# Kernel optimization log

Hardware: AMD Instinct MI355X
Metric: run time of the kernel (lower is better)

## Reference

```python
import jax, jax.numpy as jnp
import numpy as np

FEATURE_COUNT = 40960
HIDDEN = 256
BATCH = 131072
BAG = 32  # active features per perspective (fixed-size bag)


def setup_inputs() -> dict:
    key = jax.random.key(0)
    ks = jax.random.split(key, 9)
    inp = {
        "indices_us": jax.random.randint(ks[0], (BATCH, BAG), 0, FEATURE_COUNT, dtype=jnp.int32),
        "indices_them": jax.random.randint(ks[1], (BATCH, BAG), 0, FEATURE_COUNT, dtype=jnp.int32),
        "emb_weight": jax.random.normal(ks[2], (FEATURE_COUNT, HIDDEN), dtype=jnp.float32) * 0.05,
        "l1_w": jax.random.normal(ks[3], (32, 2 * HIDDEN), dtype=jnp.float32) * 0.05,
        "l1_b": jax.random.normal(ks[4], (32,), dtype=jnp.float32) * 0.05,
        "l2_w": jax.random.normal(ks[5], (32, 32), dtype=jnp.float32) * 0.05,
        "l2_b": jax.random.normal(ks[6], (32,), dtype=jnp.float32) * 0.05,
        "out_w": jax.random.normal(ks[7], (1, 32), dtype=jnp.float32) * 0.05,
        "out_b": jax.random.normal(ks[8], (1,), dtype=jnp.float32) * 0.05,
    }
    return inp


def _clipped_relu(x):
    return jnp.clip(x, 0.0, 1.0)


def reference(indices_us, indices_them, emb_weight, l1_w, l1_b, l2_w, l2_b, out_w, out_b):
    # EmbeddingBag(mode='sum') with uniform bags of size BAG:
    # gather [B, BAG, H] then sum over bag dim -> [B, H]
    acc_us = emb_weight[indices_us].sum(axis=1)
    acc_them = emb_weight[indices_them].sum(axis=1)
    x = jnp.concatenate([acc_us, acc_them], axis=1)  # [B, 2H]
    x = _clipped_relu(x)
    x = _clipped_relu(x @ l1_w.T + l1_b)
    x = _clipped_relu(x @ l2_w.T + l2_b)
    return x @ out_w.T + out_b  # [B, 1]
```

## Files before the change

kernel.cpp:

```cpp
#include <hip/hip_runtime.h>
#include <hip/hip_fp16.h>


constexpr int kBatch  = 131072;
constexpr int kHidden = 256;
constexpr int kBag    = 32;
constexpr int kFeat   = 40960;

__device__ __forceinline__ float clip1(float x) {
  return fminf(fmaxf(x, 0.0f), 1.0f);
}

template <int D, int HALF>
__device__ __forceinline__ void rs_stage(float (&p)[32], int lane) {
  const bool up = (lane & D) != 0;
#pragma unroll
  for (int i = 0; i < HALF; ++i) {
    const float send = up ? p[i] : p[i + HALF];
    const float recv = __shfl_xor(send, D, 64);
    p[i] = (up ? p[i + HALF] : p[i]) + recv;
  }
}

__device__ __forceinline__ float reduce32(float (&p)[32], int lane) {
  rs_stage<32, 16>(p, lane);
  rs_stage<16, 8>(p, lane);
  rs_stage<8, 4>(p, lane);
  rs_stage<4, 2>(p, lane);
  rs_stage<2, 1>(p, lane);
  return p[0] + __shfl_xor(p[0], 1, 64);
}

__global__ void cvt_emb(const float4* __restrict__ src, uint2* __restrict__ dst) {
  const int n4 = kFeat * kHidden / 4;
  const int stride = gridDim.x * blockDim.x;
  for (int i = blockIdx.x * blockDim.x + threadIdx.x; i < n4; i += stride) {
    const float4 v = src[i];
    union { __half2 h[2]; uint2 u; } P;
    P.h[0] = __floats2half2_rn(v.x, v.y);
    P.h[1] = __floats2half2_rn(v.z, v.w);
    dst[i] = P.u;
  }
}

constexpr int kBlocksH = 1024;
constexpr int kTpb     = 256;
constexpr int kWpb     = kTpb / 64;
constexpr int kElemsH  = kBatch / (kBlocksH * kWpb);
static_assert(kBatch % (kBlocksH * kWpb) == 0);

__device__ __forceinline__ void acc8(float (&a)[8], const uint4 v) {
  union { uint4 u; __half2 h[4]; } U;
  U.u = v;
#pragma unroll
  for (int q = 0; q < 4; ++q) {
    const float2 f = __half22float2(U.h[q]);
    a[2 * q + 0] += f.x;
    a[2 * q + 1] += f.y;
  }
}

__global__ __launch_bounds__(kTpb, 4) void nnue_fwd_h(
    const int* __restrict__ idx_us, const int* __restrict__ idx_th,
    const __half* __restrict__ embh, const float* __restrict__ w1,
    const float* __restrict__ b1, const float* __restrict__ w2,
    const float* __restrict__ b2, const float* __restrict__ wo,
    const float* __restrict__ bo, float* __restrict__ out) {
  __shared__ __align__(16) __half sW1h[32 * 512];
  __shared__ __align__(16) float sY1[kWpb][32];

  const int t = threadIdx.x;
  {
    const float4* src = (const float4*)w1;
#pragma unroll
    for (int c = 0; c < 16; ++c) {
      const float4 v = src[t * 16 + c];
      __half2* d = (__half2*)&sW1h[t * 64 + 4 * c];
      d[0] = __floats2half2_rn(v.x, v.y);
      d[1] = __floats2half2_rn(v.z, v.w);
    }
  }
  __syncthreads();

  const int lane   = t & 63;
  const int wlocal = t >> 6;
  const int wid    = blockIdx.x * kWpb + wlocal;
  const int myj    = lane >> 1;
  const int j2     = lane & 31;
  const int half31 = lane & 31;
  const bool hiHalf = lane >= 32;

  const float b1r  = b1[myj];
  const float b2r  = b2[j2];
  const float wor  = wo[j2];
  const float outb = bo[0];
  float w2r[32];
#pragma unroll
  for (int k = 0; k < 32; ++k) w2r[k] = w2[j2 * 32 + k];

  for (int e = 0; e < kElemsH; ++e) {
    const int b = wid * kElemsH + e;

    const int* ip = (lane < kBag) ? (idx_us + (size_t)b * kBag + lane)
                                  : (idx_th + (size_t)b * kBag + (lane - kBag));
    const int vidx = *ip;

    float aU[8] = {0, 0, 0, 0, 0, 0, 0, 0};
    float aT[8] = {0, 0, 0, 0, 0, 0, 0, 0};
#pragma unroll
    for (int s = 0; s < 16; ++s) {
      const int rA = __builtin_amdgcn_readlane(vidx, 2 * s);
      const int rB = __builtin_amdgcn_readlane(vidx, 2 * s + 1);
      const int row = hiHalf ? rB : rA;
      const uint4 v = ((const uint4*)embh)[row * 32 + half31];
      acc8(aU, v);
    }
#pragma unroll
    for (int s = 0; s < 16; ++s) {
      const int rA = __builtin_amdgcn_readlane(vidx, 32 + 2 * s);
      const int rB = __builtin_amdgcn_readlane(vidx, 33 + 2 * s);
      const int row = hiHalf ? rB : rA;
      const uint4 v = ((const uint4*)embh)[row * 32 + half31];
      acc8(aT, v);
    }
#pragma unroll
    for (int k = 0; k < 8; ++k) {
      aU[k] += __shfl_xor(aU[k], 32, 64);
      aT[k] += __shfl_xor(aT[k], 32, 64);
    }

    float x8[8];
#pragma unroll
    for (int k = 0; k < 8; ++k) x8[k] = clip1(hiHalf ? aT[k] : aU[k]);

    float p[32];
#pragma unroll
    for (int j = 0; j < 32; ++j) {
      const uint4 wv = *(const uint4*)&sW1h[(j * 64 + lane) * 8];
      union { uint4 u; __half2 h[4]; } W;
      W.u = wv;
      float s = 0.f;
#pragma unroll
      for (int q = 0; q < 4; ++q) {
        const float2 f = __half22float2(W.h[q]);
        s += f.x * x8[2 * q] + f.y * x8[2 * q + 1];
      }
      p[j] = s;
    }
    const float y1 = clip1(reduce32(p, lane) + b1r);

    if ((lane & 1) == 0) sY1[wlocal][myj] = y1;
    asm volatile("s_waitcnt lgkmcnt(0)" ::: "memory");

    const float4* y4 = (const float4*)&sY1[wlocal][0];
    float y2 = b2r;
#pragma unroll
    for (int k4 = 0; k4 < 8; ++k4) {
      const float4 y = y4[k4];
      y2 += w2r[4 * k4 + 0] * y.x + w2r[4 * k4 + 1] * y.y +
            w2r[4 * k4 + 2] * y.z + w2r[4 * k4 + 3] * y.w;
    }
    y2 = clip1(y2);

    float acc = y2 * wor;
#pragma unroll
    for (int d = 1; d < 32; d <<= 1) acc += __shfl_xor(acc, d, 64);
    if (lane == 0) out[b] = acc + outb;
  }
}

constexpr int kBlocksF = 512;
constexpr int kElemsF  = kBatch / (kBlocksF * kWpb);

__global__ __launch_bounds__(kTpb, 2) void nnue_fwd_f32(
    const int* __restrict__ idx_us, const int* __restrict__ idx_th,
    const float* __restrict__ emb, const float* __restrict__ w1,
    const float* __restrict__ b1, const float* __restrict__ w2,
    const float* __restrict__ b2, const float* __restrict__ wo,
    const float* __restrict__ bo, float* __restrict__ out) {
  __shared__ float sW1[32][512];
  __shared__ __align__(16) float sY1[kWpb][32];

  const int t = threadIdx.x;
  {
    const float4* src = (const float4*)w1;
    float4* dst = (float4*)&sW1[0][0];
#pragma unroll
    for (int i = 0; i < 16; ++i) dst[i * kTpb + t] = src[i * kTpb + t];
  }
  __syncthreads();

  const int lane   = t & 63;
  const int wlocal = t >> 6;
  const int wid    = blockIdx.x * kWpb + wlocal;
  const int myj    = lane >> 1;
  const int j2     = lane & 31;

  const float b1r  = b1[myj];
  const float b2r  = b2[j2];
  const float wor  = wo[j2];
  const float outb = bo[0];
  float w2r[32];
#pragma unroll
  for (int k = 0; k < 32; ++k) w2r[k] = w2[j2 * 32 + k];

  for (int e = 0; e < kElemsF; ++e) {
    const int b = wid * kElemsF + e;
    const int* ip = (lane < kBag) ? (idx_us + (size_t)b * kBag + lane)
                                  : (idx_th + (size_t)b * kBag + (lane - kBag));
    const int vidx = *ip;

    float4 au = make_float4(0.f, 0.f, 0.f, 0.f);
    float4 at = make_float4(0.f, 0.f, 0.f, 0.f);
#pragma unroll
    for (int i = 0; i < kBag; ++i) {
      const int iu = __builtin_amdgcn_readlane(vidx, i);
      const float4 v = ((const float4*)(emb + (size_t)iu * kHidden))[lane];
      au.x += v.x; au.y += v.y; au.z += v.z; au.w += v.w;
    }
#pragma unroll
    for (int i = 0; i < kBag; ++i) {
      const int it2 = __builtin_amdgcn_readlane(vidx, i + kBag);
      const float4 v = ((const float4*)(emb + (size_t)it2 * kHidden))[lane];
      at.x += v.x; at.y += v.y; at.z += v.z; at.w += v.w;
    }

    au.x = clip1(au.x); au.y = clip1(au.y); au.z = clip1(au.z); au.w = clip1(au.w);
    at.x = clip1(at.x); at.y = clip1(at.y); at.z = clip1(at.z); at.w = clip1(at.w);

    float p[32];
#pragma unroll
    for (int j = 0; j < 32; ++j) {
      const float4 a = *(const float4*)&sW1[j][4 * lane];
      const float4 c = *(const float4*)&sW1[j][kHidden + 4 * lane];
      p[j] = au.x * a.x + au.y * a.y + au.z * a.z + au.w * a.w +
             at.x * c.x + at.y * c.y + at.z * c.z + at.w * c.w;
    }
    const float y1 = clip1(reduce32(p, lane) + b1r);

    if ((lane & 1) == 0) sY1[wlocal][myj] = y1;
    asm volatile("s_waitcnt lgkmcnt(0)" ::: "memory");

    const float4* y4 = (const float4*)&sY1[wlocal][0];
    float y2 = b2r;
#pragma unroll
    for (int k4 = 0; k4 < 8; ++k4) {
      const float4 y = y4[k4];
      y2 += w2r[4 * k4 + 0] * y.x + w2r[4 * k4 + 1] * y.y +
            w2r[4 * k4 + 2] * y.z + w2r[4 * k4 + 3] * y.w;
    }
    y2 = clip1(y2);

    float acc = y2 * wor;
#pragma unroll
    for (int d = 1; d < 32; d <<= 1) acc += __shfl_xor(acc, d, 64);
    if (lane == 0) out[b] = acc + outb;
  }
}

extern "C" void kernel_launch(void* const* d_in, const int* in_sizes, int n_in,
                              void* d_out, int out_size, void* d_ws, size_t ws_size,
                              hipStream_t stream) {
  const int* idx_us  = (const int*)d_in[0];
  const int* idx_th  = (const int*)d_in[1];
  const float* emb   = (const float*)d_in[2];
  const float* w1    = (const float*)d_in[3];
  const float* b1    = (const float*)d_in[4];
  const float* w2    = (const float*)d_in[5];
  const float* b2    = (const float*)d_in[6];
  const float* wo    = (const float*)d_in[7];
  const float* bo    = (const float*)d_in[8];
  float* out         = (float*)d_out;

  const size_t embh_bytes = (size_t)kFeat * kHidden * sizeof(__half);
  if (ws_size >= embh_bytes) {
    __half* embh = (__half*)d_ws;
    cvt_emb<<<2048, 256, 0, stream>>>((const float4*)emb, (uint2*)embh);
    nnue_fwd_h<<<kBlocksH, kTpb, 0, stream>>>(idx_us, idx_th, embh, w1, b1, w2,
                                              b2, wo, bo, out);
  } else {
    nnue_fwd_f32<<<kBlocksF, kTpb, 0, stream>>>(idx_us, idx_th, emb, w1, b1,
                                                w2, b2, wo, bo, out);
  }
}
```

Before: 498.1 us.

## Use packed fp16 accumulation and fdot2 for embedding sum and dense layers

Accumulates the embedding-bag sums with packed half2 adds instead of converting each element to fp32, applies clipping with packed fp16 min/max, and computes layer 1 and layer 2 with v_dot2 fp16 instructions. The block size is raised to 512 threads with a higher occupancy hint, and the fallback f32 kernel gets its own block constants. This is meant to cut ALU instruction count in the gather and matvec phases. In exchange it accepts lower accumulation precision in fp16 and tighter register budgets that may spill.

```diff
diff --git a/kernel.cpp b/kernel.cpp
--- a/kernel.cpp
+++ b/kernel.cpp
@@ -9,6 +9,29 @@
 
 __device__ __forceinline__ float clip1(float x) {
   return fminf(fmaxf(x, 0.0f), 1.0f);
+}
+
+typedef _Float16 h2_t __attribute__((ext_vector_type(2)));
+
+__device__ __forceinline__ unsigned pkadd(unsigned a, unsigned b) {
+  const h2_t r = __builtin_bit_cast(h2_t, a) + __builtin_bit_cast(h2_t, b);
+  return __builtin_bit_cast(unsigned, r);
+}
+
+__device__ __forceinline__ unsigned pkclip(unsigned a) {
+  unsigned r;
+  const unsigned zero = 0u;
+  const unsigned one  = 0x3C003C00u;
+  asm("v_pk_max_f16 %0, %1, %2\n\t"
+      "v_pk_min_f16 %0, %0, %3"
+      : "=&v"(r)
+      : "v"(a), "v"(zero), "v"(one));
+  return r;
+}
+
+__device__ __forceinline__ float fdot2w(unsigned a, unsigned b, float c) {
+  return __builtin_amdgcn_fdot2(__builtin_bit_cast(h2_t, a),
+                                __builtin_bit_cast(h2_t, b), c, false);
 }
 
 template <int D, int HALF>
@@ -44,59 +67,51 @@
 }
 
 constexpr int kBlocksH = 1024;
-constexpr int kTpb     = 256;
+constexpr int kTpb     = 512;
 constexpr int kWpb     = kTpb / 64;
 constexpr int kElemsH  = kBatch / (kBlocksH * kWpb);
 static_assert(kBatch % (kBlocksH * kWpb) == 0);
 
-__device__ __forceinline__ void acc8(float (&a)[8], const uint4 v) {
-  union { uint4 u; __half2 h[4]; } U;
-  U.u = v;
-#pragma unroll
-  for (int q = 0; q < 4; ++q) {
-    const float2 f = __half22float2(U.h[q]);
-    a[2 * q + 0] += f.x;
-    a[2 * q + 1] += f.y;
-  }
-}
-
-__global__ __launch_bounds__(kTpb, 4) void nnue_fwd_h(
+__global__ __launch_bounds__(kTpb, 6) void nnue_fwd_h(
     const int* __restrict__ idx_us, const int* __restrict__ idx_th,
     const __half* __restrict__ embh, const float* __restrict__ w1,
     const float* __restrict__ b1, const float* __restrict__ w2,
     const float* __restrict__ b2, const float* __restrict__ wo,
     const float* __restrict__ bo, float* __restrict__ out) {
   __shared__ __align__(16) __half sW1h[32 * 512];
-  __shared__ __align__(16) float sY1[kWpb][32];
+  __shared__ __align__(16) __half sY1h[kWpb][32];
 
   const int t = threadIdx.x;
   {
     const float4* src = (const float4*)w1;
 #pragma unroll
-    for (int c = 0; c < 16; ++c) {
-      const float4 v = src[t * 16 + c];
-      __half2* d = (__half2*)&sW1h[t * 64 + 4 * c];
+    for (int c = 0; c < 8; ++c) {
+      const float4 v = src[t * 8 + c];
+      __half2* d = (__half2*)&sW1h[t * 32 + 4 * c];
       d[0] = __floats2half2_rn(v.x, v.y);
       d[1] = __floats2half2_rn(v.z, v.w);
     }
   }
   __syncthreads();
 
-  const int lane   = t & 63;
-  const int wlocal = t >> 6;
-  const int wid    = blockIdx.x * kWpb + wlocal;
-  const int myj    = lane >> 1;
-  const int j2     = lane & 31;
-  const int half31 = lane & 31;
+  const int lane    = t & 63;
+  const int wlocal  = t >> 6;
+  const int wid     = blockIdx.x * kWpb + wlocal;
+  const int myj     = lane >> 1;
+  const int j2      = lane & 31;
+  const int half31  = lane & 31;
   const bool hiHalf = lane >= 32;
 
   const float b1r  = b1[myj];
   const float b2r  = b2[j2];
   const float wor  = wo[j2];
   const float outb = bo[0];
-  float w2r[32];
-#pragma unroll
-  for (int k = 0; k < 32; ++k) w2r[k] = w2[j2 * 32 + k];
+  unsigned w2h[16];
+#pragma unroll
+  for (int k = 0; k < 16; ++k) {
+    w2h[k] = __builtin_bit_cast(
+        unsigned, __floats2half2_rn(w2[j2 * 32 + 2 * k], w2[j2 * 32 + 2 * k + 1]));
+  }
 
   for (int e = 0; e < kElemsH; ++e) {
     const int b = wid * kElemsH + e;
@@ -105,15 +120,19 @@
                                   : (idx_th + (size_t)b * kBag + (lane - kBag));
     const int vidx = *ip;
 
-    float aU[8] = {0, 0, 0, 0, 0, 0, 0, 0};
-    float aT[8] = {0, 0, 0, 0, 0, 0, 0, 0};
+    unsigned aU[8] = {0, 0, 0, 0, 0, 0, 0, 0};
+    unsigned aT[8] = {0, 0, 0, 0, 0, 0, 0, 0};
 #pragma unroll
     for (int s = 0; s < 16; ++s) {
       const int rA = __builtin_amdgcn_readlane(vidx, 2 * s);
       const int rB = __builtin_amdgcn_readlane(vidx, 2 * s + 1);
       const int row = hiHalf ? rB : rA;
       const uint4 v = ((const uint4*)embh)[row * 32 + half31];
-      acc8(aU, v);
+      const int o = (s & 1) * 4;
+      aU[o + 0] = pkadd(aU[o + 0], v.x);
+      aU[o + 1] = pkadd(aU[o + 1], v.y);
+      aU[o + 2] = pkadd(aU[o + 2], v.z);
+      aU[o + 3] = pkadd(aU[o + 3], v.w);
     }
 #pragma unroll
     for (int s = 0; s < 16; ++s) {
@@ -121,44 +140,47 @@
       const int rB = __builtin_amdgcn_readlane(vidx, 33 + 2 * s);
       const int row = hiHalf ? rB : rA;
       const uint4 v = ((const uint4*)embh)[row * 32 + half31];
-      acc8(aT, v);
-    }
-#pragma unroll
-    for (int k = 0; k < 8; ++k) {
-      aU[k] += __shfl_xor(aU[k], 32, 64);
-      aT[k] += __shfl_xor(aT[k], 32, 64);
-    }
-
-    float x8[8];
-#pragma unroll
-    for (int k = 0; k < 8; ++k) x8[k] = clip1(hiHalf ? aT[k] : aU[k]);
+      const int o = (s & 1) * 4;
+      aT[o + 0] = pkadd(aT[o + 0], v.x);
+      aT[o + 1] = pkadd(aT[o + 1], v.y);
+      aT[o + 2] = pkadd(aT[o + 2], v.z);
+      aT[o + 3] = pkadd(aT[o + 3], v.w);
+    }
+
+    unsigned x2[4];
+#pragma unroll
+    for (int q = 0; q < 4; ++q) {
+      unsigned u = pkadd(aU[q], aU[q + 4]);
+      unsigned v = pkadd(aT[q], aT[q + 4]);
+      u = pkadd(u, (unsigned)__shfl_xor((int)u, 32, 64));
+      v = pkadd(v, (unsigned)__shfl_xor((int)v, 32, 64));
+      x2[q] = pkclip(hiHalf ? v : u);
+    }
 
     float p[32];
 #pragma unroll
     for (int j = 0; j < 32; ++j) {
       const uint4 wv = *(const uint4*)&sW1h[(j * 64 + lane) * 8];
-      union { uint4 u; __half2 h[4]; } W;
-      W.u = wv;
-      float s = 0.f;
-#pragma unroll
-      for (int q = 0; q < 4; ++q) {
-        const float2 f = __half22float2(W.h[q]);
-        s += f.x * x8[2 * q] + f.y * x8[2 * q + 1];
-      }
+      float s = fdot2w(wv.x, x2[0], 0.0f);
+      s = fdot2w(wv.y, x2[1], s);
+      s = fdot2w(wv.z, x2[2], s);
+      s = fdot2w(wv.w, x2[3], s);
       p[j] = s;
     }
     const float y1 = clip1(reduce32(p, lane) + b1r);
 
-    if ((lane & 1) == 0) sY1[wlocal][myj] = y1;
+    if ((lane & 1) == 0) sY1h[wlocal][myj] = __float2half(y1);
     asm volatile("s_waitcnt lgkmcnt(0)" ::: "memory");
 
-    const float4* y4 = (const float4*)&sY1[wlocal][0];
+    const uint4* yv = (const uint4*)&sY1h[wlocal][0];
     float y2 = b2r;
 #pragma unroll
-    for (int k4 = 0; k4 < 8; ++k4) {
-      const float4 y = y4[k4];
-      y2 += w2r[4 * k4 + 0] * y.x + w2r[4 * k4 + 1] * y.y +
-            w2r[4 * k4 + 2] * y.z + w2r[4 * k4 + 3] * y.w;
+    for (int k4 = 0; k4 < 4; ++k4) {
+      const uint4 y = yv[k4];
+      y2 = fdot2w(w2h[4 * k4 + 0], y.x, y2);
+      y2 = fdot2w(w2h[4 * k4 + 1], y.y, y2);
+      y2 = fdot2w(w2h[4 * k4 + 2], y.z, y2);
+      y2 = fdot2w(w2h[4 * k4 + 3], y.w, y2);
     }
     y2 = clip1(y2);
 
@@ -169,30 +191,32 @@
   }
 }
 
+constexpr int kTpbF    = 256;
+constexpr int kWpbF    = kTpbF / 64;
 constexpr int kBlocksF = 512;
-constexpr int kElemsF  = kBatch / (kBlocksF * kWpb);
-
-__global__ __launch_bounds__(kTpb, 2) void nnue_fwd_f32(
+constexpr int kElemsF  = kBatch / (kBlocksF * kWpbF);
+
+__global__ __launch_bounds__(kTpbF, 2) void nnue_fwd_f32(
     const int* __restrict__ idx_us, const int* __restrict__ idx_th,
     const float* __restrict__ emb, const float* __restrict__ w1,
     const float* __restrict__ b1, const float* __restrict__ w2,
     const float* __restrict__ b2, const float* __restrict__ wo,
     const float* __restrict__ bo, float* __restrict__ out) {
   __shared__ float sW1[32][512];
-  __shared__ __align__(16) float sY1[kWpb][32];
+  __shared__ __align__(16) float sY1[kWpbF][32];
 
   const int t = threadIdx.x;
   {
     const float4* src = (const float4*)w1;
     float4* dst = (float4*)&sW1[0][0];
 #pragma unroll
-    for (int i = 0; i < 16; ++i) dst[i * kTpb + t] = src[i * kTpb + t];
+    for (int i = 0; i < 16; ++i) dst[i * kTpbF + t] = src[i * kTpbF + t];
   }
   __syncthreads();
 
   const int lane   = t & 63;
   const int wlocal = t >> 6;
-  const int wid    = blockIdx.x * kWpb + wlocal;
+  const int wid    = blockIdx.x * kWpbF + wlocal;
   const int myj    = lane >> 1;
   const int j2     = lane & 31;
 
@@ -279,7 +303,7 @@
     nnue_fwd_h<<<kBlocksH, kTpb, 0, stream>>>(idx_us, idx_th, embh, w1, b1, w2,
                                               b2, wo, bo, out);
   } else {
-    nnue_fwd_f32<<<kBlocksF, kTpb, 0, stream>>>(idx_us, idx_th, emb, w1, b1,
-                                                w2, b2, wo, bo, out);
-  }
-}
+    nnue_fwd_f32<<<kBlocksF, kTpbF, 0, stream>>>(idx_us, idx_th, emb, w1, b1,
+                                                 w2, b2, wo, bo, out);
+  }
+}
```

New measurement: 566.4 us. +13.7%, slower.
